# Kernel tuning notes

Hardware: AMD Instinct MI355X
Metric: run time of the kernel (lower is better)

## Reference

```python
import jax, jax.numpy as jnp
import numpy as np
from jax import lax

B_SZ, L, D_MODEL = 2, 2048, 1024
D_INNER, D_STATE, D_CONV, DT_RANK = 2048, 16, 4, 64


def setup_inputs() -> dict:
    key = jax.random.key(0)
    ks = jax.random.split(key, 9)
    s = 0.02
    x = jax.random.normal(ks[0], (B_SZ, L, D_MODEL), dtype=jnp.float32)
    W_in = jax.random.normal(ks[1], (D_MODEL, 2 * D_INNER), dtype=jnp.float32) * s
    conv_w = jax.random.normal(ks[2], (D_INNER, D_CONV), dtype=jnp.float32) * s
    conv_b = jax.random.normal(ks[3], (D_INNER,), dtype=jnp.float32) * s
    W_x = jax.random.normal(ks[4], (D_INNER, DT_RANK + 2 * D_STATE), dtype=jnp.float32) * s
    W_dt = jax.random.normal(ks[5], (DT_RANK, D_INNER), dtype=jnp.float32) * s
    b_dt = jax.random.normal(ks[6], (D_INNER,), dtype=jnp.float32) * s
    A_log = jnp.log(jnp.broadcast_to(jnp.arange(1, D_STATE + 1, dtype=jnp.float32), (D_INNER, D_STATE)))
    D = jnp.ones((D_INNER,), dtype=jnp.float32)
    W_out = jax.random.normal(ks[7], (D_INNER, D_MODEL), dtype=jnp.float32) * s
    return {"x": x, "W_in": W_in, "conv_w": conv_w, "conv_b": conv_b,
            "W_x": W_x, "W_dt": W_dt, "b_dt": b_dt, "A_log": A_log, "D": D, "W_out": W_out}


def _silu(v):
    return v * jax.nn.sigmoid(v)


def _mamba_fwd(x, W_in, conv_w, conv_b, W_x, W_dt, b_dt, A_log, D, W_out):
    b, l, _ = x.shape
    xz = x @ W_in                                  # [b,l,2*d_inner]
    xs, res = jnp.split(xz, 2, axis=-1)
    # causal depthwise conv1d (torch pads d_conv-1 both sides then truncates to l -> left pad only)
    xc = xs.transpose(0, 2, 1)                     # [b,d_inner,l]
    xc = lax.conv_general_dilated(
        xc, conv_w[:, None, :], window_strides=(1,),
        padding=[(D_CONV - 1, 0)], feature_group_count=D_INNER,
        dimension_numbers=("NCH", "OIH", "NCH")) + conv_b[None, :, None]
    u = _silu(xc.transpose(0, 2, 1))               # [b,l,d_inner]
    # projections for delta, B, C
    x_dbl = u @ W_x                                # [b,l,dt_rank+2n]
    dt, Bm, Cm = jnp.split(x_dbl, [DT_RANK, DT_RANK + D_STATE], axis=-1)
    delta = jax.nn.softplus(dt @ W_dt + b_dt)      # [b,l,d_inner]
    A = -jnp.exp(A_log)                            # [d_inner,n]

    def step(h, inp):
        d_t, B_t, C_t, u_t = inp                   # [b,d_in],[b,n],[b,n],[b,d_in]
        dA = jnp.exp(d_t[:, :, None] * A)          # [b,d_in,n]
        h = dA * h + d_t[:, :, None] * B_t[:, None, :] * u_t[:, :, None]
        y = jnp.einsum("bdn,bn->bd", h, C_t)
        return h, y

    h0 = jnp.zeros((b, D_INNER, D_STATE), dtype=u.dtype)
    _, ys = lax.scan(step, h0, (delta.transpose(1, 0, 2), Bm.transpose(1, 0, 2),
                                Cm.transpose(1, 0, 2), u.transpose(1, 0, 2)))
    y = ys.transpose(1, 0, 2) + u * D              # [b,l,d_inner]
    y = y * _silu(res)
    return y @ W_out                               # [b,l,d_model]


def reference(x, W_in, conv_w, conv_b, W_x, W_dt, b_dt, A_log, D, W_out):
    return _mamba_fwd(x, W_in, conv_w, conv_b, W_x, W_dt, b_dt, A_log, D, W_out)
```

## Files before the change

kernel.cpp:

```cpp
#include <hip/hip_runtime.h>
#include <hip/hip_bf16.h>
#include <math.h>

#define B_SZ    2
#define LSEQ    2048
#define DMODEL  1024
#define DINNER  2048
#define DSTATE  16
#define DCONV   4
#define DTRANK  64

#define NCHUNK  64
#define CLEN    (LSEQ / NCHUNK)

#define KSPLIT  16
#define NX      96

typedef unsigned short u16;
typedef __bf16 bf16x8 __attribute__((ext_vector_type(8)));
typedef float  f32x4  __attribute__((ext_vector_type(4)));

static __device__ __forceinline__ float sigmoidf_(float x) {
    return 1.0f / (1.0f + __expf(-x));
}
static __device__ __forceinline__ u16 f2b(float f) {
    unsigned int u = __float_as_uint(f);
    u = (u + 0x7fffu + ((u >> 16) & 1u)) >> 16;
    return (u16)u;
}

__global__ __launch_bounds__(256) void cast_bf16(
    const float* __restrict__ in, u16* __restrict__ out, int n8)
{
    const int i = blockIdx.x * 256 + threadIdx.x;
    if (i >= n8) return;
    const float4* p = reinterpret_cast<const float4*>(in + (size_t)i * 8);
    float4 v0 = p[0], v1 = p[1];
    union { u16 u[8]; uint4 q; } r;
    r.u[0] = f2b(v0.x); r.u[1] = f2b(v0.y); r.u[2] = f2b(v0.z); r.u[3] = f2b(v0.w);
    r.u[4] = f2b(v1.x); r.u[5] = f2b(v1.y); r.u[6] = f2b(v1.z); r.u[7] = f2b(v1.w);
    reinterpret_cast<uint4*>(out)[i] = r.q;
}

__global__ __launch_bounds__(256) void castT_bf16(
    const float* __restrict__ in, u16* __restrict__ out, int R, int C)
{
    __shared__ float t[32][33];
    const int r0 = blockIdx.y * 32, c0 = blockIdx.x * 32;
    const int tr = threadIdx.x >> 3;
    const int tc4 = (threadIdx.x & 7) * 4;
    const float4 v = *reinterpret_cast<const float4*>(in + (size_t)(r0 + tr) * C + c0 + tc4);
    t[tr][tc4 + 0] = v.x; t[tr][tc4 + 1] = v.y; t[tr][tc4 + 2] = v.z; t[tr][tc4 + 3] = v.w;
    __syncthreads();
    union { u16 u[4]; uint2 q; } r;
    #pragma unroll
    for (int j = 0; j < 4; j++) r.u[j] = f2b(t[tc4 + j][tr]);
    *reinterpret_cast<uint2*>(out + (size_t)(c0 + tr) * R + r0 + tc4) = r.q;
}

__global__ __launch_bounds__(256) void gemm_bf16_tn(
    const u16* __restrict__ A, const u16* __restrict__ Bt,
    float* __restrict__ C, int M, int N, int K, int ldc)
{
    __shared__ u16 As[128 * 32];
    __shared__ u16 Bs[128 * 32];
    const int tid  = threadIdx.x;
    const int lane = tid & 63;
    const int wave = tid >> 6;
    const int wr = wave >> 1, wc = wave & 1;
    const int bm = blockIdx.y * 128, bn = blockIdx.x * 128;
    const int lhi = lane >> 4;
    const int llo = lane & 15;

    f32x4 acc[4][4] = {};

    for (int k0 = 0; k0 < K; k0 += 32) {
        #pragma unroll
        for (int c = 0; c < 2; ++c) {
            const int s   = c * 256 + wave * 64 + lane;
            const int row = s >> 2, seg = s & 3;
            const u16* ga = A  + (size_t)(bm + row) * K + k0 + seg * 8;
            const u16* gb = Bt + (size_t)(bn + row) * K + k0 + seg * 8;
            __builtin_amdgcn_global_load_lds(
                (const __attribute__((address_space(1))) void*)ga,
                (__attribute__((address_space(3))) void*)(As + (size_t)(c * 256 + wave * 64) * 8),
                16, 0, 0);
            __builtin_amdgcn_global_load_lds(
                (const __attribute__((address_space(1))) void*)gb,
                (__attribute__((address_space(3))) void*)(Bs + (size_t)(c * 256 + wave * 64) * 8),
                16, 0, 0);
        }
        __syncthreads();

        bf16x8 af[4], bfr[4];
        #pragma unroll
        for (int m = 0; m < 4; ++m)
            af[m] = *reinterpret_cast<const bf16x8*>(&As[(wr * 64 + m * 16 + llo) * 32 + lhi * 8]);
        #pragma unroll
        for (int n = 0; n < 4; ++n)
            bfr[n] = *reinterpret_cast<const bf16x8*>(&Bs[(wc * 64 + n * 16 + llo) * 32 + lhi * 8]);
        #pragma unroll
        for (int m = 0; m < 4; ++m)
            #pragma unroll
            for (int n = 0; n < 4; ++n)
                acc[m][n] = __builtin_amdgcn_mfma_f32_16x16x32_bf16(af[m], bfr[n], acc[m][n], 0, 0, 0);
        __syncthreads();
    }

    #pragma unroll
    for (int m = 0; m < 4; ++m) {
        const int row0 = bm + wr * 64 + m * 16 + lhi * 4;
        #pragma unroll
        for (int n = 0; n < 4; ++n) {
            const int col = bn + wc * 64 + n * 16 + llo;
            #pragma unroll
            for (int j = 0; j < 4; ++j)
                C[(size_t)(row0 + j) * ldc + col] = acc[m][n][j];
        }
    }
}

__global__ __launch_bounds__(256) void gemm3_splitk(
    const float* __restrict__ u, const float* __restrict__ Wx,
    float* __restrict__ partial)
{
    __shared__ float us[64][65];
    __shared__ float wsm[64][96];

    const int tid = threadIdx.x;
    const int r0 = blockIdx.x * 64;
    const int k0 = blockIdx.y * (DINNER / KSPLIT);

    const int orow = tid >> 2;
    const int oc0  = (tid & 3) * 24;

    float acc[24];
    #pragma unroll
    for (int j = 0; j < 24; j++) acc[j] = 0.f;

    for (int ks = 0; ks < DINNER / KSPLIT; ks += 64) {
        #pragma unroll
        for (int i = 0; i < 4; i++) {
            const int row = (tid >> 4) + i * 16;
            const int kc4 = (tid & 15) * 4;
            const float4 v = *reinterpret_cast<const float4*>(
                u + (size_t)(r0 + row) * DINNER + k0 + ks + kc4);
            us[row][kc4] = v.x; us[row][kc4+1] = v.y; us[row][kc4+2] = v.z; us[row][kc4+3] = v.w;
        }
        #pragma unroll
        for (int j = 0; j < 6; j++) {
            const int fid = tid + j * 256;
            const int kr  = fid / 24;
            const int c4  = (fid % 24) * 4;
            *reinterpret_cast<float4*>(&wsm[kr][c4]) =
                *reinterpret_cast<const float4*>(Wx + (size_t)(k0 + ks + kr) * NX + c4);
        }
        __syncthreads();

        for (int kk = 0; kk < 64; ++kk) {
            const float uv = us[orow][kk];
            #pragma unroll
            for (int j = 0; j < 24; j++)
                acc[j] = fmaf(uv, wsm[kk][oc0 + j], acc[j]);
        }
        __syncthreads();
    }

    float* pp = partial + ((size_t)blockIdx.y * (B_SZ * LSEQ) + r0 + orow) * NX + oc0;
    #pragma unroll
    for (int j = 0; j < 24; j += 4)
        *reinterpret_cast<float4*>(pp + j) = make_float4(acc[j], acc[j+1], acc[j+2], acc[j+3]);
}

__global__ __launch_bounds__(256) void gemm3_reduce(
    const float* __restrict__ partial, float* __restrict__ xdbl)
{
    const int i = blockIdx.x * 256 + threadIdx.x;
    if (i >= B_SZ * LSEQ * NX / 4) return;
    float4 s = make_float4(0.f, 0.f, 0.f, 0.f);
    #pragma unroll
    for (int p = 0; p < KSPLIT; p++) {
        const float4 v = reinterpret_cast<const float4*>(
            partial + (size_t)p * (B_SZ * LSEQ) * NX)[i];
        s.x += v.x; s.y += v.y; s.z += v.z; s.w += v.w;
    }
    reinterpret_cast<float4*>(xdbl)[i] = s;
}

#define BM  64
#define BN  64
#define BKK 16

__global__ __launch_bounds__(256) void gemm_f32(
    const float* __restrict__ A, int lda,
    const float* __restrict__ B, int ldb,
    float* __restrict__ C, int ldc,
    int M, int N, int K, int epi, const float* __restrict__ bias)
{
    __shared__ float As[BKK][BM];
    __shared__ float Bs[BKK][BN];

    const int tid = threadIdx.x;
    const int bm = blockIdx.y * BM;
    const int bn = blockIdx.x * BN;
    const int tx = tid & 15;
    const int ty = tid >> 4;
    const int arow = tid >> 2;
    const int acol = (tid & 3) << 2;
    const int brow = tid >> 4;
    const int bcol = (tid & 15) << 2;

    float acc[4][4];
    #pragma unroll
    for (int i = 0; i < 4; i++)
        #pragma unroll
        for (int j = 0; j < 4; j++) acc[i][j] = 0.f;

    for (int k0 = 0; k0 < K; k0 += BKK) {
        float4 av = make_float4(0.f, 0.f, 0.f, 0.f);
        {
            const int gr = bm + arow;
            const int gc = k0 + acol;
            if (gr < M && gc + 4 <= K)
                av = *reinterpret_cast<const float4*>(A + (size_t)gr * lda + gc);
        }
        float4 bv = make_float4(0.f, 0.f, 0.f, 0.f);
        {
            const int gr = k0 + brow;
            const int gc = bn + bcol;
            if (gr < K && gc + 4 <= N)
                bv = *reinterpret_cast<const float4*>(B + (size_t)gr * ldb + gc);
        }
        As[acol + 0][arow] = av.x;
        As[acol + 1][arow] = av.y;
        As[acol + 2][arow] = av.z;
        As[acol + 3][arow] = av.w;
        *reinterpret_cast<float4*>(&Bs[brow][bcol]) = bv;
        __syncthreads();

        #pragma unroll
        for (int k = 0; k < BKK; k++) {
            float a[4], b[4];
            #pragma unroll
            for (int i = 0; i < 4; i++) a[i] = As[k][(ty << 2) + i];
            #pragma unroll
            for (int j = 0; j < 4; j++) b[j] = Bs[k][(tx << 2) + j];
            #pragma unroll
            for (int i = 0; i < 4; i++)
                #pragma unroll
                for (int j = 0; j < 4; j++)
                    acc[i][j] = fmaf(a[i], b[j], acc[i][j]);
        }
        __syncthreads();
    }

    #pragma unroll
    for (int i = 0; i < 4; i++) {
        const int row = bm + (ty << 2) + i;
        if (row >= M) continue;
        #pragma unroll
        for (int j = 0; j < 4; j++) {
            const int col = bn + (tx << 2) + j;
            if (col >= N) continue;
            float v = acc[i][j];
            if (epi == 1) {
                v += bias[col];
                v = (v > 20.f) ? v : log1pf(__expf(v));
            }
            C[(size_t)row * ldc + col] = v;
        }
    }
}

__global__ __launch_bounds__(256) void conv_silu(
    const float* __restrict__ xz, const float* __restrict__ conv_w,
    const float* __restrict__ conv_b, float* __restrict__ u)
{
    const int idx = blockIdx.x * 256 + threadIdx.x;
    if (idx >= B_SZ * LSEQ * DINNER) return;
    const int d  = idx & (DINNER - 1);
    const int bl = idx >> 11;
    const int l  = bl & (LSEQ - 1);

    float acc = conv_b[d];
    #pragma unroll
    for (int k = 0; k < DCONV; k++) {
        const int l2 = l - (DCONV - 1) + k;
        if (l2 >= 0) {
            acc = fmaf(xz[(size_t)(bl - (DCONV - 1) + k) * (2 * DINNER) + d],
                       conv_w[d * DCONV + k], acc);
        }
    }
    u[idx] = acc * sigmoidf_(acc);
}

__global__ __launch_bounds__(256) void scan_phase1(
    const float* __restrict__ delta, const float* __restrict__ u,
    const float* __restrict__ xdbl, const float* __restrict__ A_log,
    float* __restrict__ hend, float* __restrict__ Sd)
{
    const int idx = blockIdx.x * 256 + threadIdx.x;
    if (idx >= B_SZ * DINNER * NCHUNK) return;
    const int d = idx & (DINNER - 1);
    const int c = (idx >> 11) & (NCHUNK - 1);
    const int b = idx >> 17;

    float a[DSTATE];
    #pragma unroll
    for (int n = 0; n < DSTATE; n++) a[n] = -__expf(A_log[d * DSTATE + n]);

    float h[DSTATE];
    #pragma unroll
    for (int n = 0; n < DSTATE; n++) h[n] = 0.f;
    float sd = 0.f;

    const int l0 = b * LSEQ + c * CLEN;
    for (int i = 0; i < CLEN; ++i) {
        const size_t r = (size_t)(l0 + i);
        const float dv = delta[r * DINNER + d];
        const float uv = u[r * DINNER + d];
        sd += dv;
        const float4* bp = reinterpret_cast<const float4*>(xdbl + r * NX + DTRANK);
        float Bv[DSTATE];
        {
            float4 t;
            t = bp[0]; Bv[0]=t.x; Bv[1]=t.y; Bv[2]=t.z;  Bv[3]=t.w;
            t = bp[1]; Bv[4]=t.x; Bv[5]=t.y; Bv[6]=t.z;  Bv[7]=t.w;
            t = bp[2]; Bv[8]=t.x; Bv[9]=t.y; Bv[10]=t.z; Bv[11]=t.w;
            t = bp[3]; Bv[12]=t.x; Bv[13]=t.y; Bv[14]=t.z; Bv[15]=t.w;
        }
        const float du = dv * uv;
        #pragma unroll
        for (int n = 0; n < DSTATE; n++)
            h[n] = fmaf(__expf(dv * a[n]), h[n], du * Bv[n]);
    }

    float* hp = hend + ((size_t)(b * DINNER + d) * NCHUNK + c) * DSTATE;
    #pragma unroll
    for (int n = 0; n < DSTATE; n += 4)
        *reinterpret_cast<float4*>(hp + n) = make_float4(h[n], h[n+1], h[n+2], h[n+3]);
    Sd[(size_t)(b * DINNER + d) * NCHUNK + c] = sd;
}

__global__ __launch_bounds__(256) void scan_phase2(
    float* __restrict__ hend, const float* __restrict__ Sd,
    const float* __restrict__ A_log)
{
    const int idx = blockIdx.x * 256 + threadIdx.x;
    if (idx >= B_SZ * DINNER * DSTATE) return;
    const int n = idx & (DSTATE - 1);
    const int d = (idx >> 4) & (DINNER - 1);
    const int b = idx >> 15;

    const float an = -__expf(A_log[d * DSTATE + n]);
    const size_t base = (size_t)(b * DINNER + d) * NCHUNK;
    float carry = 0.f;
    for (int c = 0; c < NCHUNK; ++c) {
        const float P = __expf(an * Sd[base + c]);
        const size_t off = (base + c) * DSTATE + n;
        const float tmp = hend[off];
        hend[off] = carry;
        carry = fmaf(P, carry, tmp);
    }
}

__global__ __launch_bounds__(256) void scan_phase3(
    const float* __restrict__ dy ,
    const float* __restrict__ u, const float* __restrict__ xdbl,
    const float* __restrict__ xz, const float* __restrict__ A_log,
    const float* __restrict__ Dp, const float* __restrict__ hin,
    u16* __restrict__ ybf)
{
    const int idx = blockIdx.x * 256 + threadIdx.x;
    if (idx >= B_SZ * DINNER * NCHUNK) return;
    const int d = idx & (DINNER - 1);
    const int c = (idx >> 11) & (NCHUNK - 1);
    const int b = idx >> 17;

    float a[DSTATE];
    #pragma unroll
    for (int n = 0; n < DSTATE; n++) a[n] = -__expf(A_log[d * DSTATE + n]);
    const float Dd = Dp[d];

    float h[DSTATE];
    {
        const float* hp = hin + ((size_t)(b * DINNER + d) * NCHUNK + c) * DSTATE;
        #pragma unroll
        for (int n = 0; n < DSTATE; n += 4) {
            float4 t = *reinterpret_cast<const float4*>(hp + n);
            h[n] = t.x; h[n+1] = t.y; h[n+2] = t.z; h[n+3] = t.w;
        }
    }

    const int l0 = b * LSEQ + c * CLEN;
    for (int i = 0; i < CLEN; ++i) {
        const size_t r = (size_t)(l0 + i);
        const float dv = dy[r * DINNER + d];
        const float uv = u[r * DINNER + d];

        const float4* bp = reinterpret_cast<const float4*>(xdbl + r * NX + DTRANK);
        float Bv[DSTATE], Cv[DSTATE];
        {
            float4 t;
            t = bp[0]; Bv[0]=t.x; Bv[1]=t.y; Bv[2]=t.z;  Bv[3]=t.w;
            t = bp[1]; Bv[4]=t.x; Bv[5]=t.y; Bv[6]=t.z;  Bv[7]=t.w;
            t = bp[2]; Bv[8]=t.x; Bv[9]=t.y; Bv[10]=t.z; Bv[11]=t.w;
            t = bp[3]; Bv[12]=t.x; Bv[13]=t.y; Bv[14]=t.z; Bv[15]=t.w;
            t = bp[4]; Cv[0]=t.x; Cv[1]=t.y; Cv[2]=t.z;  Cv[3]=t.w;
            t = bp[5]; Cv[4]=t.x; Cv[5]=t.y; Cv[6]=t.z;  Cv[7]=t.w;
            t = bp[6]; Cv[8]=t.x; Cv[9]=t.y; Cv[10]=t.z; Cv[11]=t.w;
            t = bp[7]; Cv[12]=t.x; Cv[13]=t.y; Cv[14]=t.z; Cv[15]=t.w;
        }

        const float du = dv * uv;
        float yv = 0.f;
        #pragma unroll
        for (int n = 0; n < DSTATE; n++) {
            h[n] = fmaf(__expf(dv * a[n]), h[n], du * Bv[n]);
            yv = fmaf(h[n], Cv[n], yv);
        }
        yv = fmaf(uv, Dd, yv);

        const float rv = xz[r * (2 * DINNER) + DINNER + d];
        ybf[r * DINNER + d] = f2b(yv * (rv * sigmoidf_(rv)));
    }
}

extern "C" void kernel_launch(void* const* d_in, const int* in_sizes, int n_in,
                              void* d_out, int out_size, void* d_ws, size_t ws_size,
                              hipStream_t stream) {
    const float* x      = (const float*)d_in[0];
    const float* W_in   = (const float*)d_in[1];
    const float* conv_w = (const float*)d_in[2];
    const float* conv_b = (const float*)d_in[3];
    const float* W_x    = (const float*)d_in[4];
    const float* W_dt   = (const float*)d_in[5];
    const float* b_dt   = (const float*)d_in[6];
    const float* A_log  = (const float*)d_in[7];
    const float* Dp     = (const float*)d_in[8];
    const float* W_out  = (const float*)d_in[9];
    float* out = (float*)d_out;

    float* ws   = (float*)d_ws;
    float* xz   = ws;
    float* u    = xz   + (size_t)4096 * 4096;
    float* xdbl = u    + (size_t)4096 * 2048;
    float* dy   = xdbl + (size_t)4096 * 96;
    float* hend = dy   + (size_t)4096 * 2048;
    float* Sd   = hend + (size_t)B_SZ * DINNER * NCHUNK * DSTATE;
    u16*   bfp  = (u16*)(Sd + (size_t)B_SZ * DINNER * NCHUNK);
    u16*   xbf  = bfp;
    u16*   WinT = xbf + (size_t)4096 * 1024;
    u16*   ybf  = xbf;
    u16*   WoutT = (u16*)xz;
    float* part = dy;

    const int M = B_SZ * LSEQ;
    dim3 blk(256);

    cast_bf16<<<dim3((M * DMODEL / 8) / 256), blk, 0, stream>>>(x, xbf, M * DMODEL / 8);
    castT_bf16<<<dim3((2 * DINNER) / 32, DMODEL / 32), blk, 0, stream>>>(
        W_in, WinT, DMODEL, 2 * DINNER);

    gemm_bf16_tn<<<dim3((2 * DINNER) / 128, M / 128), blk, 0, stream>>>(
        xbf, WinT, xz, M, 2 * DINNER, DMODEL, 2 * DINNER);

    conv_silu<<<dim3((M * DINNER) / 256), blk, 0, stream>>>(xz, conv_w, conv_b, u);

    gemm3_splitk<<<dim3(M / 64, KSPLIT), blk, 0, stream>>>(u, W_x, part);
    gemm3_reduce<<<dim3((M * NX / 4 + 255) / 256), blk, 0, stream>>>(part, xdbl);

    gemm_f32<<<dim3(DINNER / BN, M / BM), blk, 0, stream>>>(
        xdbl, NX, W_dt, DINNER, dy, DINNER, M, DINNER, DTRANK, 1, b_dt);

    scan_phase1<<<dim3((B_SZ * DINNER * NCHUNK) / 256), blk, 0, stream>>>(
        dy, u, xdbl, A_log, hend, Sd);
    scan_phase2<<<dim3((B_SZ * DINNER * DSTATE) / 256), blk, 0, stream>>>(
        hend, Sd, A_log);
    scan_phase3<<<dim3((B_SZ * DINNER * NCHUNK) / 256), blk, 0, stream>>>(
        dy, u, xdbl, xz, A_log, Dp, hend, ybf);

    castT_bf16<<<dim3(DMODEL / 32, DINNER / 32), blk, 0, stream>>>(
        W_out, WoutT, DINNER, DMODEL);

    gemm_bf16_tn<<<dim3(DMODEL / 128, M / 128), blk, 0, stream>>>(
        ybf, WoutT, out, M, DMODEL, DINNER, DMODEL);
}
```

Before: 420.5 us.

## Store intermediates in bf16, fuse SiLU gate and delta projection into scan

The in-projection GEMM now writes its two halves as separate bf16 buffers and applies SiLU to the gate half in the epilogue. The conv now reads and writes bf16 with 8-wide vectors. The delta projection plus softplus moves into scan phase 1, which recomputes it per timestep from xdbl and writes delta in bf16 for phase 3, so the separate fp32 GEMM goes away. This aims to halve memory traffic for the large intermediates and remove one kernel launch, at the cost of bf16 rounding of u, delta and the gate, and a 64-FMA dot product per step in phase 1.

```diff
diff --git a/kernel.cpp b/kernel.cpp
--- a/kernel.cpp
+++ b/kernel.cpp
@@ -27,6 +27,9 @@
     unsigned int u = __float_as_uint(f);
     u = (u + 0x7fffu + ((u >> 16) & 1u)) >> 16;
     return (u16)u;
+}
+static __device__ __forceinline__ float b2f(u16 v) {
+    return __uint_as_float(((unsigned int)v) << 16);
 }
 
 __global__ __launch_bounds__(256) void cast_bf16(
@@ -58,9 +61,9 @@
     *reinterpret_cast<uint2*>(out + (size_t)(c0 + tr) * R + r0 + tc4) = r.q;
 }
 
-__global__ __launch_bounds__(256) void gemm_bf16_tn(
+__global__ __launch_bounds__(256) void gemm_bf16_split(
     const u16* __restrict__ A, const u16* __restrict__ Bt,
-    float* __restrict__ C, int M, int N, int K, int ldc)
+    u16* __restrict__ xs_bf, u16* __restrict__ zs_bf, int K)
 {
     __shared__ u16 As[128 * 32];
     __shared__ u16 Bs[128 * 32];
@@ -114,14 +117,123 @@
         for (int n = 0; n < 4; ++n) {
             const int col = bn + wc * 64 + n * 16 + llo;
             #pragma unroll
+            for (int j = 0; j < 4; ++j) {
+                float v = acc[m][n][j];
+                if (col < DINNER) {
+                    xs_bf[(size_t)(row0 + j) * DINNER + col] = f2b(v);
+                } else {
+                    v = v * sigmoidf_(v);
+                    zs_bf[(size_t)(row0 + j) * DINNER + (col - DINNER)] = f2b(v);
+                }
+            }
+        }
+    }
+}
+
+__global__ __launch_bounds__(256) void gemm_bf16_tn(
+    const u16* __restrict__ A, const u16* __restrict__ Bt,
+    float* __restrict__ C, int M, int N, int K, int ldc)
+{
+    __shared__ u16 As[128 * 32];
+    __shared__ u16 Bs[128 * 32];
+    const int tid  = threadIdx.x;
+    const int lane = tid & 63;
+    const int wave = tid >> 6;
+    const int wr = wave >> 1, wc = wave & 1;
+    const int bm = blockIdx.y * 128, bn = blockIdx.x * 128;
+    const int lhi = lane >> 4;
+    const int llo = lane & 15;
+
+    f32x4 acc[4][4] = {};
+
+    for (int k0 = 0; k0 < K; k0 += 32) {
+        #pragma unroll
+        for (int c = 0; c < 2; ++c) {
+            const int s   = c * 256 + wave * 64 + lane;
+            const int row = s >> 2, seg = s & 3;
+            const u16* ga = A  + (size_t)(bm + row) * K + k0 + seg * 8;
+            const u16* gb = Bt + (size_t)(bn + row) * K + k0 + seg * 8;
+            __builtin_amdgcn_global_load_lds(
+                (const __attribute__((address_space(1))) void*)ga,
+                (__attribute__((address_space(3))) void*)(As + (size_t)(c * 256 + wave * 64) * 8),
+                16, 0, 0);
+            __builtin_amdgcn_global_load_lds(
+                (const __attribute__((address_space(1))) void*)gb,
+                (__attribute__((address_space(3))) void*)(Bs + (size_t)(c * 256 + wave * 64) * 8),
+                16, 0, 0);
+        }
+        __syncthreads();
+
+        bf16x8 af[4], bfr[4];
+        #pragma unroll
+        for (int m = 0; m < 4; ++m)
+            af[m] = *reinterpret_cast<const bf16x8*>(&As[(wr * 64 + m * 16 + llo) * 32 + lhi * 8]);
+        #pragma unroll
+        for (int n = 0; n < 4; ++n)
+            bfr[n] = *reinterpret_cast<const bf16x8*>(&Bs[(wc * 64 + n * 16 + llo) * 32 + lhi * 8]);
+        #pragma unroll
+        for (int m = 0; m < 4; ++m)
+            #pragma unroll
+            for (int n = 0; n < 4; ++n)
+                acc[m][n] = __builtin_amdgcn_mfma_f32_16x16x32_bf16(af[m], bfr[n], acc[m][n], 0, 0, 0);
+        __syncthreads();
+    }
+
+    #pragma unroll
+    for (int m = 0; m < 4; ++m) {
+        const int row0 = bm + wr * 64 + m * 16 + lhi * 4;
+        #pragma unroll
+        for (int n = 0; n < 4; ++n) {
+            const int col = bn + wc * 64 + n * 16 + llo;
+            #pragma unroll
             for (int j = 0; j < 4; ++j)
                 C[(size_t)(row0 + j) * ldc + col] = acc[m][n][j];
         }
     }
 }
 
+__global__ __launch_bounds__(256) void conv_silu_bf(
+    const u16* __restrict__ xs, const float* __restrict__ conv_w,
+    const float* __restrict__ conv_b, u16* __restrict__ u)
+{
+    const int g  = blockIdx.x * 256 + threadIdx.x;
+    const int d8 = (g & 255) * 8;
+    const int bl = g >> 8;
+    const int l  = bl & (LSEQ - 1);
+
+    float4 wv[8];
+    #pragma unroll
+    for (int j = 0; j < 8; j++)
+        wv[j] = *reinterpret_cast<const float4*>(conv_w + (size_t)(d8 + j) * DCONV);
+
+    float acc[8];
+    #pragma unroll
+    for (int j = 0; j < 8; j++) acc[j] = conv_b[d8 + j];
+
+    #pragma unroll
+    for (int k = 0; k < DCONV; k++) {
+        const int l2 = l - (DCONV - 1) + k;
+        if (l2 < 0) continue;
+        const uint4 q = *reinterpret_cast<const uint4*>(
+            xs + (size_t)(bl - (DCONV - 1) + k) * DINNER + d8);
+        const u16* e = reinterpret_cast<const u16*>(&q);
+        #pragma unroll
+        for (int j = 0; j < 8; j++) {
+            const float w = (k == 0) ? wv[j].x : (k == 1) ? wv[j].y : (k == 2) ? wv[j].z : wv[j].w;
+            acc[j] = fmaf(b2f(e[j]), w, acc[j]);
+        }
+    }
+    union { u16 u[8]; uint4 q; } r;
+    #pragma unroll
+    for (int j = 0; j < 8; j++) {
+        const float v = acc[j];
+        r.u[j] = f2b(v * sigmoidf_(v));
+    }
+    *reinterpret_cast<uint4*>(u + (size_t)bl * DINNER + d8) = r.q;
+}
+
 __global__ __launch_bounds__(256) void gemm3_splitk(
-    const float* __restrict__ u, const float* __restrict__ Wx,
+    const u16* __restrict__ ubf, const float* __restrict__ Wx,
     float* __restrict__ partial)
 {
     __shared__ float us[64][65];
@@ -139,13 +251,18 @@
     for (int j = 0; j < 24; j++) acc[j] = 0.f;
 
     for (int ks = 0; ks < DINNER / KSPLIT; ks += 64) {
-        #pragma unroll
-        for (int i = 0; i < 4; i++) {
-            const int row = (tid >> 4) + i * 16;
-            const int kc4 = (tid & 15) * 4;
-            const float4 v = *reinterpret_cast<const float4*>(
-                u + (size_t)(r0 + row) * DINNER + k0 + ks + kc4);
-            us[row][kc4] = v.x; us[row][kc4+1] = v.y; us[row][kc4+2] = v.z; us[row][kc4+3] = v.w;
+        {
+            const int row = tid >> 2;
+            const int c16 = (tid & 3) << 4;
+            const uint4* src = reinterpret_cast<const uint4*>(
+                ubf + (size_t)(r0 + row) * DINNER + k0 + ks + c16);
+            const uint4 q0 = src[0], q1 = src[1];
+            const u16* e0 = reinterpret_cast<const u16*>(&q0);
+            const u16* e1 = reinterpret_cast<const u16*>(&q1);
+            #pragma unroll
+            for (int j = 0; j < 8; j++) us[row][c16 + j]     = b2f(e0[j]);
+            #pragma unroll
+            for (int j = 0; j < 8; j++) us[row][c16 + 8 + j] = b2f(e1[j]);
         }
         #pragma unroll
         for (int j = 0; j < 6; j++) {
@@ -187,124 +304,22 @@
     reinterpret_cast<float4*>(xdbl)[i] = s;
 }
 
-#define BM  64
-#define BN  64
-#define BKK 16
-
-__global__ __launch_bounds__(256) void gemm_f32(
-    const float* __restrict__ A, int lda,
-    const float* __restrict__ B, int ldb,
-    float* __restrict__ C, int ldc,
-    int M, int N, int K, int epi, const float* __restrict__ bias)
-{
-    __shared__ float As[BKK][BM];
-    __shared__ float Bs[BKK][BN];
-
-    const int tid = threadIdx.x;
-    const int bm = blockIdx.y * BM;
-    const int bn = blockIdx.x * BN;
-    const int tx = tid & 15;
-    const int ty = tid >> 4;
-    const int arow = tid >> 2;
-    const int acol = (tid & 3) << 2;
-    const int brow = tid >> 4;
-    const int bcol = (tid & 15) << 2;
-
-    float acc[4][4];
-    #pragma unroll
-    for (int i = 0; i < 4; i++)
-        #pragma unroll
-        for (int j = 0; j < 4; j++) acc[i][j] = 0.f;
-
-    for (int k0 = 0; k0 < K; k0 += BKK) {
-        float4 av = make_float4(0.f, 0.f, 0.f, 0.f);
-        {
-            const int gr = bm + arow;
-            const int gc = k0 + acol;
-            if (gr < M && gc + 4 <= K)
-                av = *reinterpret_cast<const float4*>(A + (size_t)gr * lda + gc);
-        }
-        float4 bv = make_float4(0.f, 0.f, 0.f, 0.f);
-        {
-            const int gr = k0 + brow;
-            const int gc = bn + bcol;
-            if (gr < K && gc + 4 <= N)
-                bv = *reinterpret_cast<const float4*>(B + (size_t)gr * ldb + gc);
-        }
-        As[acol + 0][arow] = av.x;
-        As[acol + 1][arow] = av.y;
-        As[acol + 2][arow] = av.z;
-        As[acol + 3][arow] = av.w;
-        *reinterpret_cast<float4*>(&Bs[brow][bcol]) = bv;
-        __syncthreads();
-
-        #pragma unroll
-        for (int k = 0; k < BKK; k++) {
-            float a[4], b[4];
-            #pragma unroll
-            for (int i = 0; i < 4; i++) a[i] = As[k][(ty << 2) + i];
-            #pragma unroll
-            for (int j = 0; j < 4; j++) b[j] = Bs[k][(tx << 2) + j];
-            #pragma unroll
-            for (int i = 0; i < 4; i++)
-                #pragma unroll
-                for (int j = 0; j < 4; j++)
-                    acc[i][j] = fmaf(a[i], b[j], acc[i][j]);
-        }
-        __syncthreads();
-    }
-
-    #pragma unroll
-    for (int i = 0; i < 4; i++) {
-        const int row = bm + (ty << 2) + i;
-        if (row >= M) continue;
-        #pragma unroll
-        for (int j = 0; j < 4; j++) {
-            const int col = bn + (tx << 2) + j;
-            if (col >= N) continue;
-            float v = acc[i][j];
-            if (epi == 1) {
-                v += bias[col];
-                v = (v > 20.f) ? v : log1pf(__expf(v));
-            }
-            C[(size_t)row * ldc + col] = v;
-        }
-    }
-}
-
-__global__ __launch_bounds__(256) void conv_silu(
-    const float* __restrict__ xz, const float* __restrict__ conv_w,
-    const float* __restrict__ conv_b, float* __restrict__ u)
+__global__ __launch_bounds__(256) void scan_phase1(
+    const u16* __restrict__ ubf, const float* __restrict__ xdbl,
+    const float* __restrict__ Wdt, const float* __restrict__ bdt,
+    const float* __restrict__ A_log,
+    float* __restrict__ hend, float* __restrict__ Sd, u16* __restrict__ delta_bf)
 {
     const int idx = blockIdx.x * 256 + threadIdx.x;
-    if (idx >= B_SZ * LSEQ * DINNER) return;
-    const int d  = idx & (DINNER - 1);
-    const int bl = idx >> 11;
-    const int l  = bl & (LSEQ - 1);
-
-    float acc = conv_b[d];
-    #pragma unroll
-    for (int k = 0; k < DCONV; k++) {
-        const int l2 = l - (DCONV - 1) + k;
-        if (l2 >= 0) {
-            acc = fmaf(xz[(size_t)(bl - (DCONV - 1) + k) * (2 * DINNER) + d],
-                       conv_w[d * DCONV + k], acc);
-        }
-    }
-    u[idx] = acc * sigmoidf_(acc);
-}
-
-__global__ __launch_bounds__(256) void scan_phase1(
-    const float* __restrict__ delta, const float* __restrict__ u,
-    const float* __restrict__ xdbl, const float* __restrict__ A_log,
-    float* __restrict__ hend, float* __restrict__ Sd)
-{
-    const int idx = blockIdx.x * 256 + threadIdx.x;
-    if (idx >= B_SZ * DINNER * NCHUNK) return;
     const int d = idx & (DINNER - 1);
     const int c = (idx >> 11) & (NCHUNK - 1);
     const int b = idx >> 17;
 
+    float w[DTRANK];
+    #pragma unroll
+    for (int k = 0; k < DTRANK; k++) w[k] = Wdt[(size_t)k * DINNER + d];
+    const float bb = bdt[d];
+
     float a[DSTATE];
     #pragma unroll
     for (int n = 0; n < DSTATE; n++) a[n] = -__expf(A_log[d * DSTATE + n]);
@@ -317,17 +332,31 @@
     const int l0 = b * LSEQ + c * CLEN;
     for (int i = 0; i < CLEN; ++i) {
         const size_t r = (size_t)(l0 + i);
-        const float dv = delta[r * DINNER + d];
-        const float uv = u[r * DINNER + d];
+        const float* xr = xdbl + r * NX;
+
+        float t = bb;
+        #pragma unroll
+        for (int k = 0; k < DTRANK; k += 4) {
+            const float4 v = *reinterpret_cast<const float4*>(xr + k);
+            t = fmaf(w[k],     v.x, t);
+            t = fmaf(w[k + 1], v.y, t);
+            t = fmaf(w[k + 2], v.z, t);
+            t = fmaf(w[k + 3], v.w, t);
+        }
+        const float dv = (t > 20.f) ? t : log1pf(__expf(t));
         sd += dv;
-        const float4* bp = reinterpret_cast<const float4*>(xdbl + r * NX + DTRANK);
+        delta_bf[r * DINNER + d] = f2b(dv);
+
+        const float uv = b2f(ubf[r * DINNER + d]);
+
         float Bv[DSTATE];
         {
-            float4 t;
-            t = bp[0]; Bv[0]=t.x; Bv[1]=t.y; Bv[2]=t.z;  Bv[3]=t.w;
-            t = bp[1]; Bv[4]=t.x; Bv[5]=t.y; Bv[6]=t.z;  Bv[7]=t.w;
-            t = bp[2]; Bv[8]=t.x; Bv[9]=t.y; Bv[10]=t.z; Bv[11]=t.w;
-            t = bp[3]; Bv[12]=t.x; Bv[13]=t.y; Bv[14]=t.z; Bv[15]=t.w;
+            const float4* bp = reinterpret_cast<const float4*>(xr + DTRANK);
+            float4 q;
+            q = bp[0]; Bv[0]=q.x;  Bv[1]=q.y;  Bv[2]=q.z;  Bv[3]=q.w;
+            q = bp[1]; Bv[4]=q.x;  Bv[5]=q.y;  Bv[6]=q.z;  Bv[7]=q.w;
+            q = bp[2]; Bv[8]=q.x;  Bv[9]=q.y;  Bv[10]=q.z; Bv[11]=q.w;
+            q = bp[3]; Bv[12]=q.x; Bv[13]=q.y; Bv[14]=q.z; Bv[15]=q.w;
         }
         const float du = dv * uv;
         #pragma unroll
@@ -365,14 +394,12 @@
 }
 
 __global__ __launch_bounds__(256) void scan_phase3(
-    const float* __restrict__ dy ,
-    const float* __restrict__ u, const float* __restrict__ xdbl,
-    const float* __restrict__ xz, const float* __restrict__ A_log,
-    const float* __restrict__ Dp, const float* __restrict__ hin,
-    u16* __restrict__ ybf)
+    const u16* __restrict__ delta_bf, const u16* __restrict__ ubf,
+    const u16* __restrict__ zs_bf, const float* __restrict__ xdbl,
+    const float* __restrict__ A_log, const float* __restrict__ Dp,
+    const float* __restrict__ hin, u16* __restrict__ ybf)
 {
     const int idx = blockIdx.x * 256 + threadIdx.x;
-    if (idx >= B_SZ * DINNER * NCHUNK) return;
     const int d = idx & (DINNER - 1);
     const int c = (idx >> 11) & (NCHUNK - 1);
     const int b = idx >> 17;
@@ -387,7 +414,7 @@
         const float* hp = hin + ((size_t)(b * DINNER + d) * NCHUNK + c) * DSTATE;
         #pragma unroll
         for (int n = 0; n < DSTATE; n += 4) {
-            float4 t = *reinterpret_cast<const float4*>(hp + n);
+            const float4 t = *reinterpret_cast<const float4*>(hp + n);
             h[n] = t.x; h[n+1] = t.y; h[n+2] = t.z; h[n+3] = t.w;
         }
     }
@@ -395,20 +422,20 @@
     const int l0 = b * LSEQ + c * CLEN;
     for (int i = 0; i < CLEN; ++i) {
         const size_t r = (size_t)(l0 + i);
-        const float dv = dy[r * DINNER + d];
-        const float uv = u[r * DINNER + d];
+        const float dv = b2f(delta_bf[r * DINNER + d]);
+        const float uv = b2f(ubf[r * DINNER + d]);
 
         const float4* bp = reinterpret_cast<const float4*>(xdbl + r * NX + DTRANK);
         float Bv[DSTATE], Cv[DSTATE];
         {
             float4 t;
-            t = bp[0]; Bv[0]=t.x; Bv[1]=t.y; Bv[2]=t.z;  Bv[3]=t.w;
-            t = bp[1]; Bv[4]=t.x; Bv[5]=t.y; Bv[6]=t.z;  Bv[7]=t.w;
-            t = bp[2]; Bv[8]=t.x; Bv[9]=t.y; Bv[10]=t.z; Bv[11]=t.w;
+            t = bp[0]; Bv[0]=t.x;  Bv[1]=t.y;  Bv[2]=t.z;  Bv[3]=t.w;
+            t = bp[1]; Bv[4]=t.x;  Bv[5]=t.y;  Bv[6]=t.z;  Bv[7]=t.w;
+            t = bp[2]; Bv[8]=t.x;  Bv[9]=t.y;  Bv[10]=t.z; Bv[11]=t.w;
             t = bp[3]; Bv[12]=t.x; Bv[13]=t.y; Bv[14]=t.z; Bv[15]=t.w;
-            t = bp[4]; Cv[0]=t.x; Cv[1]=t.y; Cv[2]=t.z;  Cv[3]=t.w;
-            t = bp[5]; Cv[4]=t.x; Cv[5]=t.y; Cv[6]=t.z;  Cv[7]=t.w;
-            t = bp[6]; Cv[8]=t.x; Cv[9]=t.y; Cv[10]=t.z; Cv[11]=t.w;
+            t = bp[4]; Cv[0]=t.x;  Cv[1]=t.y;  Cv[2]=t.z;  Cv[3]=t.w;
+            t = bp[5]; Cv[4]=t.x;  Cv[5]=t.y;  Cv[6]=t.z;  Cv[7]=t.w;
+            t = bp[6]; Cv[8]=t.x;  Cv[9]=t.y;  Cv[10]=t.z; Cv[11]=t.w;
             t = bp[7]; Cv[12]=t.x; Cv[13]=t.y; Cv[14]=t.z; Cv[15]=t.w;
         }
 
@@ -421,8 +448,8 @@
         }
         yv = fmaf(uv, Dd, yv);
 
-        const float rv = xz[r * (2 * DINNER) + DINNER + d];
-        ybf[r * DINNER + d] = f2b(yv * (rv * sigmoidf_(rv)));
+        const float g = b2f(zs_bf[r * DINNER + d]);
+        ybf[r * DINNER + d] = f2b(yv * g);
     }
 }
 
@@ -441,44 +468,43 @@
     const float* W_out  = (const float*)d_in[9];
     float* out = (float*)d_out;
 
-    float* ws   = (float*)d_ws;
-    float* xz   = ws;
-    float* u    = xz   + (size_t)4096 * 4096;
-    float* xdbl = u    + (size_t)4096 * 2048;
-    float* dy   = xdbl + (size_t)4096 * 96;
-    float* hend = dy   + (size_t)4096 * 2048;
-    float* Sd   = hend + (size_t)B_SZ * DINNER * NCHUNK * DSTATE;
-    u16*   bfp  = (u16*)(Sd + (size_t)B_SZ * DINNER * NCHUNK);
-    u16*   xbf  = bfp;
-    u16*   WinT = xbf + (size_t)4096 * 1024;
-    u16*   ybf  = xbf;
-    u16*   WoutT = (u16*)xz;
-    float* part = dy;
-
     const int M = B_SZ * LSEQ;
+
+    float* ws    = (float*)d_ws;
+    float* xdbl  = ws;
+    float* hend  = xdbl + (size_t)M * NX;
+    float* Sd    = hend + (size_t)B_SZ * DINNER * NCHUNK * DSTATE;
+    float* part  = Sd   + (size_t)B_SZ * DINNER * NCHUNK;
+    u16*   xs_bf = (u16*)(part + (size_t)KSPLIT * M * NX);
+    u16*   zs_bf = xs_bf + (size_t)M * DINNER;
+    u16*   u_bf  = zs_bf + (size_t)M * DINNER;
+    u16*   dl_bf = u_bf  + (size_t)M * DINNER;
+    u16*   xbf   = dl_bf + (size_t)M * DINNER;
+    u16*   WinT  = xbf   + (size_t)M * DMODEL;
+    u16*   WoutT = WinT  + (size_t)M * DMODEL;
+    u16*   ybf   = xbf;
+
     dim3 blk(256);
 
     cast_bf16<<<dim3((M * DMODEL / 8) / 256), blk, 0, stream>>>(x, xbf, M * DMODEL / 8);
     castT_bf16<<<dim3((2 * DINNER) / 32, DMODEL / 32), blk, 0, stream>>>(
         W_in, WinT, DMODEL, 2 * DINNER);
 
-    gemm_bf16_tn<<<dim3((2 * DINNER) / 128, M / 128), blk, 0, stream>>>(
-        xbf, WinT, xz, M, 2 * DINNER, DMODEL, 2 * DINNER);
-
-    conv_silu<<<dim3((M * DINNER) / 256), blk, 0, stream>>>(xz, conv_w, conv_b, u);
-
-    gemm3_splitk<<<dim3(M / 64, KSPLIT), blk, 0, stream>>>(u, W_x, part);
+    gemm_bf16_split<<<dim3((2 * DINNER) / 128, M / 128), blk, 0, stream>>>(
+        xbf, WinT, xs_bf, zs_bf, DMODEL);
+
+    conv_silu_bf<<<dim3((M * DINNER / 8) / 256), blk, 0, stream>>>(
+        xs_bf, conv_w, conv_b, u_bf);
+
+    gemm3_splitk<<<dim3(M / 64, KSPLIT), blk, 0, stream>>>(u_bf, W_x, part);
     gemm3_reduce<<<dim3((M * NX / 4 + 255) / 256), blk, 0, stream>>>(part, xdbl);
 
-    gemm_f32<<<dim3(DINNER / BN, M / BM), blk, 0, stream>>>(
-        xdbl, NX, W_dt, DINNER, dy, DINNER, M, DINNER, DTRANK, 1, b_dt);
-
     scan_phase1<<<dim3((B_SZ * DINNER * NCHUNK) / 256), blk, 0, stream>>>(
-        dy, u, xdbl, A_log, hend, Sd);
+        u_bf, xdbl, W_dt, b_dt, A_log, hend, Sd, dl_bf);
     scan_phase2<<<dim3((B_SZ * DINNER * DSTATE) / 256), blk, 0, stream>>>(
         hend, Sd, A_log);
     scan_phase3<<<dim3((B_SZ * DINNER * NCHUNK) / 256), blk, 0, stream>>>(
-        dy, u, xdbl, xz, A_log, Dp, hend, ybf);
+        dl_bf, u_bf, zs_bf, xdbl, A_log, Dp, hend, ybf);
 
     castT_bf16<<<dim3(DMODEL / 32, DINNER / 32), blk, 0, stream>>>(
         W_out, WoutT, DINNER, DMODEL);
```

Measured after the change: 441.2 us. 1.05x slower.
